# Optimization experiments

Measured on AMD Instinct MI355X. Metric: run time of the kernel, lower is better.

The kernel has to match this reference:

```python
import jax, jax.numpy as jnp
import numpy as np

NUM_USERS = 100000
NUM_ITEMS = 50000
NUM_EDGES = 2000000
DIM = 64
NUM_REL = 5


def setup_inputs() -> dict:
    key = jax.random.key(0)
    k1, k2, k3, k4, k5, k6 = jax.random.split(key, 6)
    u_features = jax.random.normal(k1, (NUM_USERS, DIM), dtype=jnp.float32)
    i_features = jax.random.normal(k2, (NUM_ITEMS, DIM), dtype=jnp.float32)
    edge_user = jax.random.randint(k3, (NUM_EDGES,), 0, NUM_USERS, dtype=jnp.int64)
    edge_item = jax.random.randint(k4, (NUM_EDGES,), 0, NUM_ITEMS, dtype=jnp.int64)
    # per-relation Linear params, torch convention: y = x @ W[r].T + b[r]
    W = jax.random.normal(k5, (NUM_REL, DIM, DIM), dtype=jnp.float32) * (1.0 / np.sqrt(DIM))
    b = jax.random.normal(k6, (NUM_REL, DIM), dtype=jnp.float32) * 0.01
    return {"u_features": u_features, "i_features": i_features,
            "edge_user": edge_user, "edge_item": edge_item, "W": W, "b": b}


def reference(u_features, i_features, edge_user, edge_item, W, b):
    # gather edge endpoint features: [E, D]
    edge_u = u_features[edge_user]
    edge_i = i_features[edge_item]
    num_rel = W.shape[0]
    # per relation: sum((edge_u @ W[r].T + b[r]) * edge_i, axis=1) -> [E]
    # loop over small fixed relation count to avoid [E, R, D] intermediate
    cols = [jnp.sum((edge_u @ W[r].T + b[r]) * edge_i, axis=1)
            for r in range(num_rel)]
    return jnp.stack(cols, axis=1)  # [E, R]
```

## Files before the change

kernel.cpp:

```cpp
#include <hip/hip_runtime.h>
#include <stdint.h>

#define NREL 5
#define D 64
#define Q_BYTES 320
#define NT 21
#define NB 8
#define CHUNK 4096
#define EDGE_GRID 2048

typedef __attribute__((ext_vector_type(8))) short short8;
typedef __attribute__((ext_vector_type(4))) float f32x4;

static __device__ __forceinline__ short f2bf(float f) {
    uint32_t u = __float_as_uint(f);
    u += 0x7FFFu + ((u >> 16) & 1u);
    return (short)(u >> 16);
}

#if defined(__has_builtin)
#if __has_builtin(__builtin_amdgcn_sdot4)
#define HAVE_SDOT4 1
#endif
#endif
#ifdef HAVE_SDOT4
static __device__ __forceinline__ int SDOT4(uint32_t a, uint32_t b, int c) {
    return __builtin_amdgcn_sdot4((int)a, (int)b, c, false);
}
#else
static __device__ __forceinline__ int SDOT4(uint32_t a, uint32_t b, int c) {
    c += ((int)(a << 24) >> 24) * ((int)(b << 24) >> 24);
    c += ((int)(a << 16) >> 24) * ((int)(b << 16) >> 24);
    c += ((int)(a << 8) >> 24) * ((int)(b << 8) >> 24);
    c += ((int)a >> 24) * ((int)b >> 24);
    return c;
}
#endif

__global__ __launch_bounds__(256) void wprep_kernel(
    const float* __restrict__ W, const float* __restrict__ bias_p, short* __restrict__ Wf,
    int* __restrict__ totals)
{
    if (blockIdx.x == 0 && threadIdx.x < NB) totals[threadIdx.x] = 0;
    const int tid = blockIdx.x * 256 + threadIdx.x;
    if (tid >= NT * 2 * 64) return;
    const int lane = tid & 63;
    const int h = (tid >> 6) & 1;
    const int nt = tid >> 7;
    const int ln = lane & 15, quad = lane >> 4;
    const int n = nt * 16 + ln;
    uint32_t w[4];
#pragma unroll
    for (int p = 0; p < 4; ++p) {
        uint32_t lo = 0, hi = 0;
#pragma unroll
        for (int s = 0; s < 2; ++s) {
            const int j = p * 2 + s;
            const int d = h * 32 + quad * 8 + j;
            float v;
            if (nt < 20) v = W[(n >> 6) * (D * D) + d * D + (n & 63)];
            else         v = (ln < NREL) ? bias_p[ln * D + d] : 0.f;
            if (s == 0) lo = (uint16_t)f2bf(v); else hi = (uint16_t)f2bf(v);
        }
        w[p] = lo | (hi << 16);
    }
    *(uint4*)(Wf + (size_t)tid * 8) = make_uint4(w[0], w[1], w[2], w[3]);
}

__global__ __launch_bounds__(256) void fused_kernel(
    const float* __restrict__ i_feat, const short* __restrict__ Wf,
    char* __restrict__ qrecs, float* __restrict__ sc, int nItems,
    const float* __restrict__ uf, uint32_t* __restrict__ uq,
    float* __restrict__ uscale, int nUsers,
    const int* __restrict__ edge_user, const int* __restrict__ edge_item,
    int nE, int bucketDiv, int cap,
    int* __restrict__ totals, uint32_t* __restrict__ sorted,
    uint16_t* __restrict__ perm, int* __restrict__ blockBase)
{
    __shared__ int cnt[NB];
    __shared__ int base[NB];
    const int nbI = (nItems + 63) / 64;
    const int nbS = (nE + CHUNK - 1) / CHUNK;
    int bid = blockIdx.x;

    if (bid < nbI) {
        const int lane = threadIdx.x & 63;
        const int wv = threadIdx.x >> 6;
        const int m0 = bid * 64 + wv * 16;
        const int ln = lane & 15, quad = lane >> 4;

        int rowA = m0 + ln;
        if (rowA >= nItems) rowA = nItems - 1;
        const float* ap = i_feat + (size_t)rowA * D + quad * 8;
        short8 af[2];
#pragma unroll
        for (int h = 0; h < 2; ++h) {
            const float4 x = *(const float4*)(ap + h * 32);
            const float4 y = *(const float4*)(ap + h * 32 + 4);
            short8 a;
            a[0] = f2bf(x.x); a[1] = f2bf(x.y); a[2] = f2bf(x.z); a[3] = f2bf(x.w);
            a[4] = f2bf(y.x); a[5] = f2bf(y.y); a[6] = f2bf(y.z); a[7] = f2bf(y.w);
            af[h] = a;
        }

        f32x4 acc[NT];
#pragma unroll
        for (int nt = 0; nt < NT; ++nt) acc[nt] = (f32x4){0.f, 0.f, 0.f, 0.f};

#pragma unroll
        for (int nt = 0; nt < NT; ++nt) {
            const short8 b0 = *(const short8*)(Wf + ((size_t)(nt * 2 + 0) * 64 + lane) * 8);
            acc[nt] = __builtin_amdgcn_mfma_f32_16x16x32_bf16(af[0], b0, acc[nt], 0, 0, 0);
            const short8 b1 = *(const short8*)(Wf + ((size_t)(nt * 2 + 1) * 64 + lane) * 8);
            acc[nt] = __builtin_amdgcn_mfma_f32_16x16x32_bf16(af[1], b1, acc[nt], 0, 0, 0);
        }

#pragma unroll
        for (int g = 0; g < 4; ++g) {
            const int item = m0 + quad * 4 + g;
            const bool ok = (item < nItems);
            char* rec = qrecs + (size_t)item * Q_BYTES;
#pragma unroll
            for (int r = 0; r < NREL; ++r) {
                const float v0 = acc[4 * r + 0][g];
                const float v1 = acc[4 * r + 1][g];
                const float v2 = acc[4 * r + 2][g];
                const float v3 = acc[4 * r + 3][g];
                float m = fmaxf(fmaxf(fabsf(v0), fabsf(v1)), fmaxf(fabsf(v2), fabsf(v3)));
                m = fmaxf(m, __shfl_xor(m, 1));
                m = fmaxf(m, __shfl_xor(m, 2));
                m = fmaxf(m, __shfl_xor(m, 4));
                m = fmaxf(m, __shfl_xor(m, 8));
                m = fmaxf(m, 1e-20f);
                const float qs = 127.0f / m;
                const uint32_t pw = ((uint32_t)(uint8_t)(int8_t)(int)rintf(v0 * qs))
                                  | ((uint32_t)(uint8_t)(int8_t)(int)rintf(v1 * qs) << 8)
                                  | ((uint32_t)(uint8_t)(int8_t)(int)rintf(v2 * qs) << 16)
                                  | ((uint32_t)(uint8_t)(int8_t)(int)rintf(v3 * qs) << 24);
                if (ok) {
                    *(uint32_t*)(rec + r * D + ln * 4) = pw;
                    if (ln == 0) sc[(size_t)item * 16 + 2 * r] = m * (1.0f / 127.0f);
                }
            }
            if (ok && ln < NREL) sc[(size_t)item * 16 + 2 * ln + 1] = acc[20][g];
        }
        return;
    }
    bid -= nbI;

    if (bid < nbS) {
        if (threadIdx.x < NB) cnt[threadIdx.x] = 0;
        __syncthreads();

        const long start = (long)bid * CHUNK;
        uint32_t pk[CHUNK / 256];
        unsigned long long bins = 0;
        unsigned long long accLo = 0, accHi = 0;
#pragma unroll
        for (int k = 0; k < CHUNK / 256; ++k) {
            const long e = start + k * 256 + threadIdx.x;
            const bool ok = (e < nE);
            int iu = 0, ii = 0;
            if (ok) { iu = edge_user[e]; ii = edge_item[e]; }
            const int bn = ok ? (ii / bucketDiv) : 0;
            const int iiL = ii - bn * bucketDiv;
            pk[k] = ok ? ((uint32_t)iu | ((uint32_t)iiL << 17)) : 0xFFFFFFFFu;
            bins |= (unsigned long long)bn << (k * 3);
            if (ok) {
                const unsigned long long one = 1ull << ((bn & 3) * 16);
                if (bn < 4) accLo += one; else accHi += one;
            }
        }
#pragma unroll
        for (int d = 1; d < 64; d <<= 1) {
            accLo += __shfl_xor(accLo, d);
            accHi += __shfl_xor(accHi, d);
        }
        if ((threadIdx.x & 63) == 0) {
#pragma unroll
            for (int f = 0; f < 4; ++f) {
                atomicAdd(&cnt[f],     (int)((accLo >> (f * 16)) & 0xFFFF));
                atomicAdd(&cnt[4 + f], (int)((accHi >> (f * 16)) & 0xFFFF));
            }
        }
        __syncthreads();
        if (threadIdx.x < NB) {
            const int c = cnt[threadIdx.x];
            const int bs = threadIdx.x * cap + atomicAdd(&totals[threadIdx.x], c);
            base[threadIdx.x] = bs;
            blockBase[bid * NB + threadIdx.x] = bs;
            cnt[threadIdx.x] = 0;
        }
        __syncthreads();
#pragma unroll
        for (int k = 0; k < CHUNK / 256; ++k) {
            if (pk[k] != 0xFFFFFFFFu) {
                const long e = start + k * 256 + threadIdx.x;
                const int bn = (int)((bins >> (k * 3)) & 7);
                const int r = atomicAdd(&cnt[bn], 1);
                sorted[base[bn] + r] = pk[k];
                perm[e] = (uint16_t)((bn << 12) | r);
            }
        }
        return;
    }
    bid -= nbS;

    const int gid = bid * 256 + threadIdx.x;
    const int row = gid >> 4;
    const int t = gid & 15;
    if (row >= nUsers) return;
    const float* rp = uf + (size_t)row * D;
    const float v0 = rp[t], v1 = rp[16 + t], v2 = rp[32 + t], v3 = rp[48 + t];
    float m = fmaxf(fmaxf(fabsf(v0), fabsf(v1)), fmaxf(fabsf(v2), fabsf(v3)));
    m = fmaxf(m, __shfl_xor(m, 1));
    m = fmaxf(m, __shfl_xor(m, 2));
    m = fmaxf(m, __shfl_xor(m, 4));
    m = fmaxf(m, __shfl_xor(m, 8));
    m = fmaxf(m, 1e-20f);
    const float qs = 127.0f / m;
    const int q0 = (int)rintf(v0 * qs);
    const int q1 = (int)rintf(v1 * qs);
    const int q2 = (int)rintf(v2 * qs);
    const int q3 = (int)rintf(v3 * qs);
    uq[(size_t)row * 16 + t] = ((uint32_t)(uint8_t)(int8_t)q0)
                             | ((uint32_t)(uint8_t)(int8_t)q1 << 8)
                             | ((uint32_t)(uint8_t)(int8_t)q2 << 16)
                             | ((uint32_t)(uint8_t)(int8_t)q3 << 24);
    if (t == 0) uscale[row] = m * (1.0f / 127.0f);
}

__global__ __launch_bounds__(256) void edge_kernel(
    const uint32_t* __restrict__ u_q,
    const float* __restrict__ u_scale,
    const uint32_t* __restrict__ sorted,
    const int* __restrict__ totals, int cap, int bucketDiv,
    const char* __restrict__ qrecs,
    const float* __restrict__ sc,
    float* __restrict__ resA,
    float* __restrict__ resB)
{
    const int b = blockIdx.x & 7;
    const int seg = blockIdx.x >> 3;
    const int nSeg = gridDim.x >> 3;
    const int s0 = b * cap;
    const int s1 = s0 + totals[b];
    const int cnt = s1 - s0;
    const int per = (cnt + nSeg - 1) / nSeg;
    const int p0 = s0 + seg * per;
    const int p1 = min(p0 + per, s1);

    const int lane = threadIdx.x & 63;
    const int wv = threadIdx.x >> 6;
    const int es = lane >> 2;
    const int c = lane & 3;
    const int itemBase = b * bucketDiv;

    for (int q0 = p0 + wv * 16; q0 < p1; q0 += 64) {
        const int pos = q0 + es;
        if (pos < p1) {
            const uint32_t pk = sorted[pos];
            const int iu = (int)(pk & 0x1FFFF);
            const int ii = itemBase + (int)(pk >> 17);

            const uint4 uv = *(const uint4*)(u_q + (size_t)iu * 16 + c * 4);
            const char* rec = qrecs + (size_t)ii * Q_BYTES;

            int s[NREL];
#pragma unroll
            for (int r = 0; r < NREL; ++r) {
                const uint4 yv = *(const uint4*)(rec + r * D + c * 16);
                int t = SDOT4(uv.x, yv.x, 0);
                t = SDOT4(uv.y, yv.y, t);
                t = SDOT4(uv.z, yv.z, t);
                s[r] = SDOT4(uv.w, yv.w, t);
            }
#pragma unroll
            for (int r = 0; r < NREL; ++r) {
                s[r] += __shfl_xor(s[r], 1);
                s[r] += __shfl_xor(s[r], 2);
            }
            const float us = u_scale[iu];
            const float* scp = sc + (size_t)ii * 16;
            const float2 sb = *(const float2*)(scp + 2 * c);
            __builtin_nontemporal_store(fmaf((float)s[c], us * sb.x, sb.y),
                                        resA + (size_t)pos * 4 + c);
            if (c == 0) {
                const float2 sb4 = *(const float2*)(scp + 8);
                __builtin_nontemporal_store(fmaf((float)s[4], us * sb4.x, sb4.y),
                                            resB + pos);
            }
        }
    }
}

__global__ __launch_bounds__(256) void unperm_kernel(
    const uint16_t* __restrict__ perm,
    const int* __restrict__ blockBase,
    const float4* __restrict__ resA,
    const float* __restrict__ resB,
    int nE,
    float* __restrict__ out)
{
    __shared__ int bb[NB];
    if (threadIdx.x < NB) bb[threadIdx.x] = blockBase[blockIdx.x * NB + threadIdx.x];
    __syncthreads();
    const long start = (long)blockIdx.x * CHUNK;
#pragma unroll
    for (int k = 0; k < CHUNK / 256; ++k) {
        const long e = start + k * 256 + threadIdx.x;
        if (e < nE) {
            const int pr = perm[e];
            const int p = bb[pr >> 12] + (pr & 0xFFF);
            const float4 a = resA[p];
            const float b5 = resB[p];
            float* op = out + e * NREL;
            op[0] = a.x; op[1] = a.y; op[2] = a.z; op[3] = a.w; op[4] = b5;
        }
    }
}

extern "C" void kernel_launch(void* const* d_in, const int* in_sizes, int n_in,
                              void* d_out, int out_size, void* d_ws, size_t ws_size,
                              hipStream_t stream) {
    const float* u_feat    = (const float*)d_in[0];
    const float* i_feat    = (const float*)d_in[1];
    const int*   edge_user = (const int*)d_in[2];
    const int*   edge_item = (const int*)d_in[3];
    const float* W         = (const float*)d_in[4];
    const float* b         = (const float*)d_in[5];
    float* out = (float*)d_out;

    const int nUsers = in_sizes[0] / D;
    const int nItems = in_sizes[1] / D;
    const int nE = in_sizes[2];
    const int bucketDiv = (nItems + NB - 1) / NB;
    const int nBlocksSort = (nE + CHUNK - 1) / CHUNK;
    const int cap = nE / NB + 4096;

    size_t off = 0;
    char* qrecs = (char*)d_ws;
    off += ((size_t)nItems * Q_BYTES + 255) & ~(size_t)255;
    float* sc = (float*)((char*)d_ws + off);
    off += ((size_t)nItems * 16 * sizeof(float) + 255) & ~(size_t)255;
    uint32_t* u_q = (uint32_t*)((char*)d_ws + off);
    off += ((size_t)nUsers * D + 255) & ~(size_t)255;
    float* u_scale = (float*)((char*)d_ws + off);
    off += ((size_t)nUsers * sizeof(float) + 255) & ~(size_t)255;
    short* Wf = (short*)((char*)d_ws + off);
    off += ((size_t)NT * 2 * 64 * 8 * sizeof(short) + 255) & ~(size_t)255;
    int* totals = (int*)((char*)d_ws + off);
    off += 256;
    int* blockBase = (int*)((char*)d_ws + off);
    off += ((size_t)nBlocksSort * NB * sizeof(int) + 255) & ~(size_t)255;
    uint32_t* sorted = (uint32_t*)((char*)d_ws + off);
    off += ((size_t)NB * cap * sizeof(uint32_t) + 255) & ~(size_t)255;
    uint16_t* perm = (uint16_t*)((char*)d_ws + off);
    off += ((size_t)nE * sizeof(uint16_t) + 255) & ~(size_t)255;
    float* resA = (float*)((char*)d_ws + off);
    off += ((size_t)NB * cap * 4 * sizeof(float) + 255) & ~(size_t)255;
    float* resB = (float*)((char*)d_ws + off);
    off += ((size_t)NB * cap * sizeof(float) + 255) & ~(size_t)255;

    wprep_kernel<<<(NT * 2 * 64 + 255) / 256, 256, 0, stream>>>(W, b, Wf, totals);

    const int nbI = (nItems + 63) / 64;
    const int nbU = (nUsers * 16 + 255) / 256;
    fused_kernel<<<nbI + nBlocksSort + nbU, 256, 0, stream>>>(
        i_feat, Wf, qrecs, sc, nItems,
        u_feat, u_q, u_scale, nUsers,
        edge_user, edge_item, nE, bucketDiv, cap,
        totals, sorted, perm, blockBase);

    edge_kernel<<<EDGE_GRID, 256, 0, stream>>>(u_q, u_scale, sorted, totals, cap, bucketDiv,
                                               qrecs, sc, resA, resB);
    unperm_kernel<<<nBlocksSort, 256, 0, stream>>>(perm, blockBase,
                                                   (const float4*)resA, resB, nE, out);
}
```

Before: 239.7 us.

## Split item MFMA transform out of the fused prep kernel, fold weight prep in

```diff
diff --git a/kernel.cpp b/kernel.cpp
--- a/kernel.cpp
+++ b/kernel.cpp
@@ -37,39 +37,8 @@
 }
 #endif
 
-__global__ __launch_bounds__(256) void wprep_kernel(
+__global__ __launch_bounds__(256) void slim_prep_kernel(
     const float* __restrict__ W, const float* __restrict__ bias_p, short* __restrict__ Wf,
-    int* __restrict__ totals)
-{
-    if (blockIdx.x == 0 && threadIdx.x < NB) totals[threadIdx.x] = 0;
-    const int tid = blockIdx.x * 256 + threadIdx.x;
-    if (tid >= NT * 2 * 64) return;
-    const int lane = tid & 63;
-    const int h = (tid >> 6) & 1;
-    const int nt = tid >> 7;
-    const int ln = lane & 15, quad = lane >> 4;
-    const int n = nt * 16 + ln;
-    uint32_t w[4];
-#pragma unroll
-    for (int p = 0; p < 4; ++p) {
-        uint32_t lo = 0, hi = 0;
-#pragma unroll
-        for (int s = 0; s < 2; ++s) {
-            const int j = p * 2 + s;
-            const int d = h * 32 + quad * 8 + j;
-            float v;
-            if (nt < 20) v = W[(n >> 6) * (D * D) + d * D + (n & 63)];
-            else         v = (ln < NREL) ? bias_p[ln * D + d] : 0.f;
-            if (s == 0) lo = (uint16_t)f2bf(v); else hi = (uint16_t)f2bf(v);
-        }
-        w[p] = lo | (hi << 16);
-    }
-    *(uint4*)(Wf + (size_t)tid * 8) = make_uint4(w[0], w[1], w[2], w[3]);
-}
-
-__global__ __launch_bounds__(256) void fused_kernel(
-    const float* __restrict__ i_feat, const short* __restrict__ Wf,
-    char* __restrict__ qrecs, float* __restrict__ sc, int nItems,
     const float* __restrict__ uf, uint32_t* __restrict__ uq,
     float* __restrict__ uscale, int nUsers,
     const int* __restrict__ edge_user, const int* __restrict__ edge_item,
@@ -79,74 +48,38 @@
 {
     __shared__ int cnt[NB];
     __shared__ int base[NB];
-    const int nbI = (nItems + 63) / 64;
+    const int nbW = (NT * 2 * 64 + 255) / 256;
     const int nbS = (nE + CHUNK - 1) / CHUNK;
     int bid = blockIdx.x;
 
-    if (bid < nbI) {
-        const int lane = threadIdx.x & 63;
-        const int wv = threadIdx.x >> 6;
-        const int m0 = bid * 64 + wv * 16;
+    if (bid < nbW) {
+        if (bid == 0 && threadIdx.x < NB) totals[threadIdx.x] = 0;
+        const int tid = bid * 256 + threadIdx.x;
+        if (tid >= NT * 2 * 64) return;
+        const int lane = tid & 63;
+        const int h = (tid >> 6) & 1;
+        const int nt = tid >> 7;
         const int ln = lane & 15, quad = lane >> 4;
-
-        int rowA = m0 + ln;
-        if (rowA >= nItems) rowA = nItems - 1;
-        const float* ap = i_feat + (size_t)rowA * D + quad * 8;
-        short8 af[2];
-#pragma unroll
-        for (int h = 0; h < 2; ++h) {
-            const float4 x = *(const float4*)(ap + h * 32);
-            const float4 y = *(const float4*)(ap + h * 32 + 4);
-            short8 a;
-            a[0] = f2bf(x.x); a[1] = f2bf(x.y); a[2] = f2bf(x.z); a[3] = f2bf(x.w);
-            a[4] = f2bf(y.x); a[5] = f2bf(y.y); a[6] = f2bf(y.z); a[7] = f2bf(y.w);
-            af[h] = a;
-        }
-
-        f32x4 acc[NT];
-#pragma unroll
-        for (int nt = 0; nt < NT; ++nt) acc[nt] = (f32x4){0.f, 0.f, 0.f, 0.f};
-
-#pragma unroll
-        for (int nt = 0; nt < NT; ++nt) {
-            const short8 b0 = *(const short8*)(Wf + ((size_t)(nt * 2 + 0) * 64 + lane) * 8);
-            acc[nt] = __builtin_amdgcn_mfma_f32_16x16x32_bf16(af[0], b0, acc[nt], 0, 0, 0);
-            const short8 b1 = *(const short8*)(Wf + ((size_t)(nt * 2 + 1) * 64 + lane) * 8);
-            acc[nt] = __builtin_amdgcn_mfma_f32_16x16x32_bf16(af[1], b1, acc[nt], 0, 0, 0);
-        }
-
-#pragma unroll
-        for (int g = 0; g < 4; ++g) {
-            const int item = m0 + quad * 4 + g;
-            const bool ok = (item < nItems);
-            char* rec = qrecs + (size_t)item * Q_BYTES;
-#pragma unroll
-            for (int r = 0; r < NREL; ++r) {
-                const float v0 = acc[4 * r + 0][g];
-                const float v1 = acc[4 * r + 1][g];
-                const float v2 = acc[4 * r + 2][g];
-                const float v3 = acc[4 * r + 3][g];
-                float m = fmaxf(fmaxf(fabsf(v0), fabsf(v1)), fmaxf(fabsf(v2), fabsf(v3)));
-                m = fmaxf(m, __shfl_xor(m, 1));
-                m = fmaxf(m, __shfl_xor(m, 2));
-                m = fmaxf(m, __shfl_xor(m, 4));
-                m = fmaxf(m, __shfl_xor(m, 8));
-                m = fmaxf(m, 1e-20f);
-                const float qs = 127.0f / m;
-                const uint32_t pw = ((uint32_t)(uint8_t)(int8_t)(int)rintf(v0 * qs))
-                                  | ((uint32_t)(uint8_t)(int8_t)(int)rintf(v1 * qs) << 8)
-                                  | ((uint32_t)(uint8_t)(int8_t)(int)rintf(v2 * qs) << 16)
-                                  | ((uint32_t)(uint8_t)(int8_t)(int)rintf(v3 * qs) << 24);
-                if (ok) {
-                    *(uint32_t*)(rec + r * D + ln * 4) = pw;
-                    if (ln == 0) sc[(size_t)item * 16 + 2 * r] = m * (1.0f / 127.0f);
-                }
-            }
-            if (ok && ln < NREL) sc[(size_t)item * 16 + 2 * ln + 1] = acc[20][g];
-        }
+        const int n = nt * 16 + ln;
+        uint32_t w[4];
+#pragma unroll
+        for (int p = 0; p < 4; ++p) {
+            uint32_t lo = 0, hi = 0;
+#pragma unroll
+            for (int s = 0; s < 2; ++s) {
+                const int j = p * 2 + s;
+                const int d = h * 32 + quad * 8 + j;
+                float v;
+                if (nt < 20) v = W[(n >> 6) * (D * D) + d * D + (n & 63)];
+                else         v = (ln < NREL) ? bias_p[ln * D + d] : 0.f;
+                if (s == 0) lo = (uint16_t)f2bf(v); else hi = (uint16_t)f2bf(v);
+            }
+            w[p] = lo | (hi << 16);
+        }
+        *(uint4*)(Wf + (size_t)tid * 8) = make_uint4(w[0], w[1], w[2], w[3]);
         return;
     }
-    bid -= nbI;
+    bid -= nbW;
 
     if (bid < nbS) {
         if (threadIdx.x < NB) cnt[threadIdx.x] = 0;
@@ -228,6 +161,75 @@
                              | ((uint32_t)(uint8_t)(int8_t)q2 << 16)
                              | ((uint32_t)(uint8_t)(int8_t)q3 << 24);
     if (t == 0) uscale[row] = m * (1.0f / 127.0f);
+}
+
+__global__ __launch_bounds__(256) void item_transform_kernel(
+    const float* __restrict__ i_feat,
+    const short* __restrict__ Wf,
+    char* __restrict__ qrecs,
+    float* __restrict__ sc,
+    int nItems)
+{
+    const int lane = threadIdx.x & 63;
+    const int wv = threadIdx.x >> 6;
+    const int m0 = blockIdx.x * 64 + wv * 16;
+    const int ln = lane & 15, quad = lane >> 4;
+
+    int rowA = m0 + ln;
+    if (rowA >= nItems) rowA = nItems - 1;
+    const float* ap = i_feat + (size_t)rowA * D + quad * 8;
+    short8 af[2];
+#pragma unroll
+    for (int h = 0; h < 2; ++h) {
+        const float4 x = *(const float4*)(ap + h * 32);
+        const float4 y = *(const float4*)(ap + h * 32 + 4);
+        short8 a;
+        a[0] = f2bf(x.x); a[1] = f2bf(x.y); a[2] = f2bf(x.z); a[3] = f2bf(x.w);
+        a[4] = f2bf(y.x); a[5] = f2bf(y.y); a[6] = f2bf(y.z); a[7] = f2bf(y.w);
+        af[h] = a;
+    }
+
+    f32x4 acc[NT];
+#pragma unroll
+    for (int nt = 0; nt < NT; ++nt) acc[nt] = (f32x4){0.f, 0.f, 0.f, 0.f};
+
+#pragma unroll
+    for (int nt = 0; nt < NT; ++nt) {
+        const short8 b0 = *(const short8*)(Wf + ((size_t)(nt * 2 + 0) * 64 + lane) * 8);
+        acc[nt] = __builtin_amdgcn_mfma_f32_16x16x32_bf16(af[0], b0, acc[nt], 0, 0, 0);
+        const short8 b1 = *(const short8*)(Wf + ((size_t)(nt * 2 + 1) * 64 + lane) * 8);
+        acc[nt] = __builtin_amdgcn_mfma_f32_16x16x32_bf16(af[1], b1, acc[nt], 0, 0, 0);
+    }
+
+#pragma unroll
+    for (int g = 0; g < 4; ++g) {
+        const int item = m0 + quad * 4 + g;
+        const bool ok = (item < nItems);
+        char* rec = qrecs + (size_t)item * Q_BYTES;
+#pragma unroll
+        for (int r = 0; r < NREL; ++r) {
+            const float v0 = acc[4 * r + 0][g];
+            const float v1 = acc[4 * r + 1][g];
+            const float v2 = acc[4 * r + 2][g];
+            const float v3 = acc[4 * r + 3][g];
+            float m = fmaxf(fmaxf(fabsf(v0), fabsf(v1)), fmaxf(fabsf(v2), fabsf(v3)));
+            m = fmaxf(m, __shfl_xor(m, 1));
+            m = fmaxf(m, __shfl_xor(m, 2));
+            m = fmaxf(m, __shfl_xor(m, 4));
+            m = fmaxf(m, __shfl_xor(m, 8));
+            m = fmaxf(m, 1e-20f);
+            const float qs = 127.0f / m;
+            const uint32_t pw = ((uint32_t)(uint8_t)(int8_t)(int)rintf(v0 * qs))
+                              | ((uint32_t)(uint8_t)(int8_t)(int)rintf(v1 * qs) << 8)
+                              | ((uint32_t)(uint8_t)(int8_t)(int)rintf(v2 * qs) << 16)
+                              | ((uint32_t)(uint8_t)(int8_t)(int)rintf(v3 * qs) << 24);
+            if (ok) {
+                *(uint32_t*)(rec + r * D + ln * 4) = pw;
+                if (ln == 0) sc[(size_t)item * 16 + 2 * r] = m * (1.0f / 127.0f);
+            }
+        }
+        if (ok && ln < NREL) sc[(size_t)item * 16 + 2 * ln + 1] = acc[20][g];
+    }
 }
 
 __global__ __launch_bounds__(256) void edge_kernel(
@@ -362,15 +364,15 @@
     float* resB = (float*)((char*)d_ws + off);
     off += ((size_t)NB * cap * sizeof(float) + 255) & ~(size_t)255;
 
-    wprep_kernel<<<(NT * 2 * 64 + 255) / 256, 256, 0, stream>>>(W, b, Wf, totals);
-
-    const int nbI = (nItems + 63) / 64;
+    const int nbW = (NT * 2 * 64 + 255) / 256;
     const int nbU = (nUsers * 16 + 255) / 256;
-    fused_kernel<<<nbI + nBlocksSort + nbU, 256, 0, stream>>>(
-        i_feat, Wf, qrecs, sc, nItems,
+    slim_prep_kernel<<<nbW + nBlocksSort + nbU, 256, 0, stream>>>(
+        W, b, Wf,
         u_feat, u_q, u_scale, nUsers,
         edge_user, edge_item, nE, bucketDiv, cap,
         totals, sorted, perm, blockBase);
+
+    item_transform_kernel<<<(nItems + 63) / 64, 256, 0, stream>>>(i_feat, Wf, qrecs, sc, nItems);
 
     edge_kernel<<<EDGE_GRID, 256, 0, stream>>>(u_q, u_scale, sorted, totals, cap, bucketDiv,
                                                qrecs, sc, resA, resB);
```

Result: no change. 243.5 us (+1.6%).
